# Kernel optimization log

Hardware: AMD Instinct MI355X
Metric: run time of the kernel (lower is better)

Reference implementation:

```python
import jax, jax.numpy as jnp
import numpy as np

B, T, N = 16, 2048, 1024
SPIKE_RATE = 0.02


def setup_inputs() -> dict:
    key = jax.random.key(0)
    k1, k2 = jax.random.split(key)
    u = jax.random.uniform(k1, (B, T, N), dtype=jnp.float32)
    output_spikes = (u < SPIKE_RATE).astype(jnp.float32)
    target_cv = jax.random.uniform(k2, (N,), dtype=jnp.float32)
    return {"output_spikes": output_spikes, "target_cv": target_cv}


def reference(output_spikes, target_cv):
    # Flatten (batch[, patterns], time) into one long trial-concatenated train per neuron,
    # matching output_spikes[:, :, n].reshape(-1) in the torch loop.
    n_neurons = output_spikes.shape[-1]
    s = output_spikes.reshape(-1, n_neurons)          # (Ttot, N)
    Ttot = s.shape[0]
    m = s > 0                                          # spike mask
    times = jnp.arange(Ttot, dtype=jnp.float32)[:, None]

    # Previous spike time at each position via exclusive cumulative max of spike times.
    st = jnp.where(m, times, -1.0)                     # (Ttot, N)
    cmax = jax.lax.cummax(st, axis=0)
    prev = jnp.concatenate([jnp.full((1, n_neurons), -1.0, st.dtype), cmax[:-1]], axis=0)

    # ISI gap at every spike that has a predecessor: gap = t - prev_spike_time.
    gmask = m & (prev >= 0.0)
    gaps = jnp.where(gmask, times - prev, 0.0)

    k = jnp.sum(m, axis=0).astype(jnp.float32)         # spike count per neuron
    n_isi = k - 1.0                                    # number of ISIs
    sum_g = jnp.sum(gaps, axis=0)
    sum_g2 = jnp.sum(gaps * gaps, axis=0)

    mean_isi = sum_g / jnp.maximum(n_isi, 1.0)
    # torch.Tensor.std is unbiased (divide by n_isi - 1)
    var = (sum_g2 - n_isi * mean_isi * mean_isi) / jnp.maximum(n_isi - 1.0, 1.0)
    std = jnp.sqrt(jnp.maximum(var, 0.0))

    # NaN in torch corresponds here to: <3 spikes or mean_isi <= 0 -> excluded from loss.
    valid = (k >= 3.0) & (mean_isi > 0.0)
    cv = jnp.where(valid, std / jnp.where(mean_isi > 0.0, mean_isi, 1.0), 0.0)
    sq = jnp.where(valid, (cv - target_cv) ** 2, 0.0)
    nvalid = jnp.sum(valid.astype(jnp.float32))
    return jnp.where(nvalid > 0.0, jnp.sum(sq) / jnp.maximum(nvalid, 1.0), 0.0)
```

## Files before the change

kernel.cpp:

```cpp
#include <hip/hip_runtime.h>
#include <math.h>

#define TTOT   32768
#define NNEUR  1024
#define NCHUNK 256
#define SUBLEN 32
#define NC4    (NNEUR / 4)

struct SegState { float cnt, first, last, g2; };

__device__ __forceinline__ SegState seg_combine(const SegState& a, const SegState& b) {
    if (a.cnt == 0.0f) return b;
    if (b.cnt == 0.0f) return a;
    SegState r;
    float gap = b.first - a.last;
    r.cnt   = a.cnt + b.cnt;
    r.first = a.first;
    r.last  = b.last;
    r.g2    = a.g2 + b.g2 + gap * gap;
    return r;
}

__global__ __launch_bounds__(256) void k_scan(const float* __restrict__ s,
                                              float4* __restrict__ wstate) {
    const int tid  = threadIdx.x;
    const int ccol = tid & 63;
    const int ysl  = tid >> 6;
    const int col4 = blockIdx.x * 64 + ccol;
    const int t0   = blockIdx.y * 128 + ysl * SUBLEN;

    const uint4* s4 = reinterpret_cast<const uint4*>(s);

    unsigned int m0 = 0u, m1 = 0u, m2 = 0u, m3 = 0u;

    for (int g = 0; g < 4; ++g) {
        uint4 v[8];
        #pragma unroll
        for (int i = 0; i < 8; ++i)
            v[i] = s4[(size_t)(t0 + g * 8 + i) * NC4 + col4];
        #pragma unroll
        for (int i = 0; i < 8; ++i) {
            const int rb = g * 8 + i;
            m0 |= ((v[i].x >> 23) & 1u) << rb;
            m1 |= ((v[i].y >> 23) & 1u) << rb;
            m2 |= ((v[i].z >> 23) & 1u) << rb;
            m3 |= ((v[i].w >> 23) & 1u) << rb;
        }
    }

    const unsigned int m[4] = {m0, m1, m2, m3};
    float cnt[4], first[4], last[4], g2[4];
    #pragma unroll
    for (int j = 0; j < 4; ++j) {
        const unsigned int mask = m[j];
        if (mask) {
            cnt[j] = (float)__popc(mask);
            const int fr = __builtin_ctz(mask);
            const int lr = 31 - __builtin_clz(mask);
            first[j] = (float)(t0 + fr);
            last[j]  = (float)(t0 + lr);
            float acc = 0.f;
            unsigned int mm = mask & (mask - 1u);
            int prevp = fr;
            while (mm) {
                const int p = __builtin_ctz(mm);
                mm &= mm - 1u;
                const int d = p - prevp;
                acc += (float)(d * d);
                prevp = p;
            }
            g2[j] = acc;
        } else {
            cnt[j] = 0.f; first[j] = -1.f; last[j] = -1.f; g2[j] = 0.f;
        }
    }

    __shared__ float4 lds[4][64][4];
    #pragma unroll
    for (int j = 0; j < 4; ++j)
        lds[ysl][ccol][j] = make_float4(cnt[j], first[j], last[j], g2[j]);
    __syncthreads();

    if (ysl == 0) {
        #pragma unroll
        for (int j = 0; j < 4; ++j) {
            float4 a = lds[0][ccol][j];
            SegState st = {a.x, a.y, a.z, a.w};
            #pragma unroll
            for (int y = 1; y < 4; ++y) {
                float4 b = lds[y][ccol][j];
                SegState sb = {b.x, b.y, b.z, b.w};
                st = seg_combine(st, sb);
            }
            wstate[(size_t)blockIdx.y * NNEUR + col4 * 4 + j] =
                make_float4(st.cnt, st.first, st.last, st.g2);
        }
    }
}

__global__ __launch_bounds__(256) void k_combine(const float4* __restrict__ wstate,
                                                 const float* __restrict__ target,
                                                 float* __restrict__ outsq,
                                                 float* __restrict__ outvalid) {
    const int tid  = threadIdx.x;
    const int lane = tid & 63;
    const int w    = tid >> 6;
    const int n    = blockIdx.x * 4 + w;

    SegState st = {0.f, -1.f, -1.f, 0.f};
    #pragma unroll
    for (int j = 0; j < NCHUNK / 64; ++j) {
        int c = lane * (NCHUNK / 64) + j;
        float4 a = wstate[(size_t)c * NNEUR + n];
        SegState sb = {a.x, a.y, a.z, a.w};
        st = seg_combine(st, sb);
    }
    for (int off = 1; off < 64; off <<= 1) {
        SegState o;
        o.cnt   = __shfl_down(st.cnt,   off);
        o.first = __shfl_down(st.first, off);
        o.last  = __shfl_down(st.last,  off);
        o.g2    = __shfl_down(st.g2,    off);
        if ((lane & (2 * off - 1)) == 0) st = seg_combine(st, o);
    }

    if (lane == 0) {
        float k     = st.cnt;
        float n_isi = k - 1.0f;
        float sum_g = (k > 0.0f) ? (st.last - st.first) : 0.0f;
        float mean  = sum_g / fmaxf(n_isi, 1.0f);
        float var   = (st.g2 - n_isi * mean * mean) / fmaxf(n_isi - 1.0f, 1.0f);
        float sd    = sqrtf(fmaxf(var, 0.0f));
        bool valid  = (k >= 3.0f) && (mean > 0.0f);
        float cv    = valid ? sd / mean : 0.0f;
        float d     = cv - target[n];
        outsq[n]    = valid ? d * d : 0.0f;
        outvalid[n] = valid ? 1.0f : 0.0f;
    }
}

__global__ __launch_bounds__(256) void k_reduce(const float* __restrict__ outsq,
                                                const float* __restrict__ outvalid,
                                                float* __restrict__ out) {
    const int tid = threadIdx.x;
    float s = 0.f, v = 0.f;
    for (int i = tid; i < NNEUR; i += 256) {
        s += outsq[i];
        v += outvalid[i];
    }
    for (int off = 32; off > 0; off >>= 1) {
        s += __shfl_down(s, off);
        v += __shfl_down(v, off);
    }
    __shared__ float ls[4], lv[4];
    const int w = tid >> 6;
    if ((tid & 63) == 0) { ls[w] = s; lv[w] = v; }
    __syncthreads();
    if (tid == 0) {
        float S = ls[0] + ls[1] + ls[2] + ls[3];
        float V = lv[0] + lv[1] + lv[2] + lv[3];
        out[0] = (V > 0.0f) ? S / fmaxf(V, 1.0f) : 0.0f;
    }
}

extern "C" void kernel_launch(void* const* d_in, const int* in_sizes, int n_in,
                              void* d_out, int out_size, void* d_ws, size_t ws_size,
                              hipStream_t stream) {
    const float* spikes = (const float*)d_in[0];
    const float* target = (const float*)d_in[1];
    float* out = (float*)d_out;

    char* wsb = (char*)d_ws;
    float4* wstate   = (float4*)wsb;
    float*  outsq    = (float*)(wsb + (size_t)NCHUNK * NNEUR * sizeof(float4));
    float*  outvalid = outsq + NNEUR;

    dim3 g1(NNEUR / 256, NCHUNK);
    k_scan<<<g1, 256, 0, stream>>>(spikes, wstate);
    k_combine<<<NNEUR / 4, 256, 0, stream>>>(wstate, target, outsq, outvalid);
    k_reduce<<<1, 256, 0, stream>>>(outsq, outvalid, out);
}
```

Baseline: 34.93 us.

## Replace LDS cross-wavefront combine in scan with intra-wave shuffles

Remaps threads so that each wavefront covers 16 column groups across four 32-row time sub-slices, instead of one sub-slice per wavefront. The per-block combine of the four sub-segments now uses two shuffle-down steps inside the wavefront, replacing the shared-memory staging and the __syncthreads barrier. This removes LDS traffic and the block barrier where three of the four wavefronts sat idle during the combine. In exchange, each wavefront's global loads now cover 16 contiguous uint4 per row across 4 rows, so a load instruction touches four row segments instead of one fully contiguous 1 KB row.

```diff
diff --git a/kernel.cpp b/kernel.cpp
--- a/kernel.cpp
+++ b/kernel.cpp
@@ -4,7 +4,6 @@
 #define TTOT   32768
 #define NNEUR  1024
 #define NCHUNK 256
-#define SUBLEN 32
 #define NC4    (NNEUR / 4)
 
 struct SegState { float cnt, first, last, g2; };
@@ -24,23 +23,25 @@
 __global__ __launch_bounds__(256) void k_scan(const float* __restrict__ s,
                                               float4* __restrict__ wstate) {
     const int tid  = threadIdx.x;
-    const int ccol = tid & 63;
-    const int ysl  = tid >> 6;
-    const int col4 = blockIdx.x * 64 + ccol;
-    const int t0   = blockIdx.y * 128 + ysl * SUBLEN;
+    const int lane = tid & 63;
+    const int w    = tid >> 6;
+    const int g    = lane >> 4;
+    const int c    = lane & 15;
+    const int col4 = blockIdx.x * 64 + w * 16 + c;
+    const int t0L  = blockIdx.y * 128 + g * 32;
 
     const uint4* s4 = reinterpret_cast<const uint4*>(s);
 
     unsigned int m0 = 0u, m1 = 0u, m2 = 0u, m3 = 0u;
 
-    for (int g = 0; g < 4; ++g) {
+    for (int b = 0; b < 4; ++b) {
         uint4 v[8];
         #pragma unroll
         for (int i = 0; i < 8; ++i)
-            v[i] = s4[(size_t)(t0 + g * 8 + i) * NC4 + col4];
+            v[i] = s4[(size_t)(t0L + b * 8 + i) * NC4 + col4];
         #pragma unroll
         for (int i = 0; i < 8; ++i) {
-            const int rb = g * 8 + i;
+            const int rb = b * 8 + i;
             m0 |= ((v[i].x >> 23) & 1u) << rb;
             m1 |= ((v[i].y >> 23) & 1u) << rb;
             m2 |= ((v[i].z >> 23) & 1u) << rb;
@@ -49,16 +50,16 @@
     }
 
     const unsigned int m[4] = {m0, m1, m2, m3};
-    float cnt[4], first[4], last[4], g2[4];
     #pragma unroll
-    for (int j = 0; j < 4; ++j) {
-        const unsigned int mask = m[j];
+    for (int k = 0; k < 4; ++k) {
+        const unsigned int mask = m[k];
+        SegState st;
         if (mask) {
-            cnt[j] = (float)__popc(mask);
+            st.cnt = (float)__popc(mask);
             const int fr = __builtin_ctz(mask);
             const int lr = 31 - __builtin_clz(mask);
-            first[j] = (float)(t0 + fr);
-            last[j]  = (float)(t0 + lr);
+            st.first = (float)(t0L + fr);
+            st.last  = (float)(t0L + lr);
             float acc = 0.f;
             unsigned int mm = mask & (mask - 1u);
             int prevp = fr;
@@ -69,32 +70,26 @@
                 acc += (float)(d * d);
                 prevp = p;
             }
-            g2[j] = acc;
+            st.g2 = acc;
         } else {
-            cnt[j] = 0.f; first[j] = -1.f; last[j] = -1.f; g2[j] = 0.f;
+            st = {0.f, -1.f, -1.f, 0.f};
         }
-    }
 
-    __shared__ float4 lds[4][64][4];
-    #pragma unroll
-    for (int j = 0; j < 4; ++j)
-        lds[ysl][ccol][j] = make_float4(cnt[j], first[j], last[j], g2[j]);
-    __syncthreads();
+        SegState o;
+        o.cnt   = __shfl_down(st.cnt,   16);
+        o.first = __shfl_down(st.first, 16);
+        o.last  = __shfl_down(st.last,  16);
+        o.g2    = __shfl_down(st.g2,    16);
+        st = seg_combine(st, o);
+        o.cnt   = __shfl_down(st.cnt,   32);
+        o.first = __shfl_down(st.first, 32);
+        o.last  = __shfl_down(st.last,  32);
+        o.g2    = __shfl_down(st.g2,    32);
+        st = seg_combine(st, o);
 
-    if (ysl == 0) {
-        #pragma unroll
-        for (int j = 0; j < 4; ++j) {
-            float4 a = lds[0][ccol][j];
-            SegState st = {a.x, a.y, a.z, a.w};
-            #pragma unroll
-            for (int y = 1; y < 4; ++y) {
-                float4 b = lds[y][ccol][j];
-                SegState sb = {b.x, b.y, b.z, b.w};
-                st = seg_combine(st, sb);
-            }
-            wstate[(size_t)blockIdx.y * NNEUR + col4 * 4 + j] =
+        if (lane < 16)
+            wstate[(size_t)blockIdx.y * NNEUR + col4 * 4 + k] =
                 make_float4(st.cnt, st.first, st.last, st.g2);
-        }
     }
 }
 
```

After: 34.79 us. Within noise of the previous version (-0.4%).
